# Kernel tuning notes

Measured on AMD Instinct MI355X. Metric: run time of the kernel, lower is better.

## Reference

```python
import jax, jax.numpy as jnp
import numpy as np

D_MODEL = 1024
NUM_HEADS = 16
HEAD_DIM = D_MODEL // NUM_HEADS  # 64
N = 1024
B = 8


def setup_inputs() -> dict:
    key = jax.random.key(0)
    ks = jax.random.split(key, 11)
    s = 0.02
    inp = {
        'query': jax.random.normal(ks[0], (B, D_MODEL, N), jnp.float32),
        'key':   jax.random.normal(ks[1], (B, D_MODEL, N), jnp.float32),
        'value': jax.random.normal(ks[2], (B, D_MODEL, N), jnp.float32),
        # 1x1 conv1d == linear over channel dim: weight [out, in], bias [out]
        'Wq': jax.random.normal(ks[3], (D_MODEL, D_MODEL), jnp.float32) * s,
        'bq': jax.random.normal(ks[4], (D_MODEL,), jnp.float32) * s,
        'Wk': jax.random.normal(ks[5], (D_MODEL, D_MODEL), jnp.float32) * s,
        'bk': jax.random.normal(ks[6], (D_MODEL,), jnp.float32) * s,
        'Wv': jax.random.normal(ks[7], (D_MODEL, D_MODEL), jnp.float32) * s,
        'bv': jax.random.normal(ks[8], (D_MODEL,), jnp.float32) * s,
        'Wm': jax.random.normal(ks[9], (D_MODEL, D_MODEL), jnp.float32) * s,
        'bm': jax.random.normal(ks[10], (D_MODEL,), jnp.float32) * s,
    }
    return inp


def _proj(W, b, x):
    # nn.Conv1d(kernel_size=1): out[b,o,n] = sum_i W[o,i] x[b,i,n] + b[o]
    return jnp.einsum('oi,bin->bon', W, x) + b[None, :, None]


def reference(query, key, value, Wq, bq, Wk, bk, Wv, bv, Wm, bm):
    Bd = query.shape[0]
    # view(B, dim, heads, N): channel axis split as (head_dim, num_heads)
    q = _proj(Wq, bq, query).reshape(Bd, HEAD_DIM, NUM_HEADS, -1)
    k = _proj(Wk, bk, key).reshape(Bd, HEAD_DIM, NUM_HEADS, -1)
    v = _proj(Wv, bv, value).reshape(Bd, HEAD_DIM, NUM_HEADS, -1)
    scale = 1.0 / (HEAD_DIM ** 0.5)
    scores = jnp.einsum('bdhn,bdhm->bhnm', q, k) * scale  # [B,H,N,N]
    prob = jax.nn.softmax(scores, axis=-1)
    x = jnp.einsum('bhnm,bdhm->bdhn', prob, v)  # [B,D,H,N]
    out = _proj(Wm, bm, x.reshape(Bd, HEAD_DIM * NUM_HEADS, -1))
    return out
```

## Files before the change

### kernel.cpp

```cpp
#include <hip/hip_runtime.h>

typedef __bf16 bf16x8 __attribute__((ext_vector_type(8)));
typedef __bf16 bf16x4 __attribute__((ext_vector_type(4)));
typedef float f32x4 __attribute__((ext_vector_type(4)));
typedef unsigned short u16;
typedef unsigned int u32;

__device__ __forceinline__ u16 f2bf(float f) {
  u32 u = __builtin_bit_cast(u32, f);
  u = (u + 0x7FFFu + ((u >> 16) & 1u)) >> 16;
  return (u16)u;
}

__device__ __forceinline__ void gload_lds16(const void* g, void* l) {
  __builtin_amdgcn_global_load_lds((const __attribute__((address_space(1))) void*)g,
                                   (__attribute__((address_space(3))) void*)l, 16, 0, 0);
}

__global__ __launch_bounds__(256) void transpose_cast(const float* __restrict__ src,
                                                      u16* __restrict__ dst) {
  __shared__ float T[64][68];
  int tid = threadIdx.x;
  int n0 = blockIdx.x * 64, i0 = blockIdx.y * 64;
  size_t boff = (size_t)blockIdx.z << 20;
  const float* s = src + boff;
  u16* d = dst + boff;
  int ir = tid >> 4, n4 = (tid & 15) * 4;
#pragma unroll
  for (int r = 0; r < 4; ++r) {
    int i_loc = ir + r * 16;
    float4 v = *(const float4*)(s + (size_t)(i0 + i_loc) * 1024 + n0 + n4);
    *(float4*)&T[i_loc][n4] = v;
  }
  __syncthreads();
  int nr = tid >> 3, i8 = (tid & 7) * 8;
#pragma unroll
  for (int r = 0; r < 2; ++r) {
    int n_loc = nr + r * 32;
    u32 pk[4];
#pragma unroll
    for (int j = 0; j < 4; ++j) {
      float f0 = T[i8 + 2 * j][n_loc];
      float f1 = T[i8 + 2 * j + 1][n_loc];
      pk[j] = (u32)f2bf(f0) | ((u32)f2bf(f1) << 16);
    }
    *(uint4*)(d + (size_t)(n0 + n_loc) * 1024 + i0 + i8) = make_uint4(pk[0], pk[1], pk[2], pk[3]);
  }
}

__global__ __launch_bounds__(256) void cast_weights(const float* __restrict__ Wq,
                                                    const float* __restrict__ Wk,
                                                    const float* __restrict__ Wv,
                                                    const float* __restrict__ Wm,
                                                    u16* __restrict__ out) {
  int w = blockIdx.y;
  const float* src = (w == 0) ? Wq : (w == 1) ? Wk : (w == 2) ? Wv : Wm;
  u16* dst = out + ((size_t)w << 20);
  int o = blockIdx.x;
  int c4 = threadIdx.x * 4;
  float f[4];
  if (w < 3) {
    float4 v = *(const float4*)(src + (size_t)o * 1024 + c4);
    f[0] = v.x; f[1] = v.y; f[2] = v.z; f[3] = v.w;
  } else {
#pragma unroll
    for (int j = 0; j < 4; ++j) {
      int cp = c4 + j;
      f[j] = src[(size_t)o * 1024 + (cp & 63) * 16 + (cp >> 6)];
    }
  }
  u32 p0 = (u32)f2bf(f[0]) | ((u32)f2bf(f[1]) << 16);
  u32 p1 = (u32)f2bf(f[2]) | ((u32)f2bf(f[3]) << 16);
  *(uint2*)(dst + (size_t)o * 1024 + c4) = make_uint2(p0, p1);
}

template <int EPI>
__global__ __launch_bounds__(512, 2) void gemm4b(const u16* __restrict__ A,
                                                 const u16* __restrict__ B,
                                                 const float* __restrict__ bias,
                                                 void* __restrict__ Out, float escale) {
  __shared__ u16 LD[49152];
  int tid = threadIdx.x;
  int wave = tid >> 6, l = tid & 63, ln = l & 15, g = l >> 4;
  int wm = wave >> 2, wn = wave & 3;
  int bid = blockIdx.x;
  int mt = (bid >> 3) & 7;
  int nt = ((bid & 7) << 2) | (bid >> 6);
  int c0 = mt * 128, n0 = nt * 256;

  int R = tid >> 3, sl = tid & 7;
  int v = sl ^ (R & 7);
  int sa = v >> 2, sg = v & 3;
  const u16* aSrc = A + (size_t)(c0 + 2 * R + sa) * 1024 + sg * 8;
  const u16* bSrc0 = B + (size_t)(n0 + 2 * R + sa) * 1024 + sg * 8;
  const u16* bSrc1 = B + (size_t)(n0 + 128 + 2 * R + sa) * 1024 + sg * 8;

  int slr = ((((ln & 1) << 2) | g) ^ ((ln >> 1) & 7)) * 8;
  int laneA = (wm * 32 + (ln >> 1)) * 64 + slr;
  int laneB = (wn * 32 + (ln >> 1)) * 64 + slr;

  f32x4 acc[4][4] = {};

#define STAGE(buf, kt)                                                   \
  do {                                                                   \
    gload_lds16(aSrc + (kt) * 32, &LD[(buf) * 4096 + tid * 8]);          \
    gload_lds16(bSrc0 + (kt) * 32, &LD[16384 + (buf) * 8192 + tid * 8]); \
    gload_lds16(bSrc1 + (kt) * 32,                                       \
                &LD[16384 + (buf) * 8192 + 4096 + tid * 8]);             \
  } while (0)

  STAGE(0, 0);
  STAGE(1, 1);
  STAGE(2, 2);

#pragma unroll
  for (int t = 0; t < 32; ++t) {
    if (t < 30)
      asm volatile("s_waitcnt vmcnt(6)" ::: "memory");
    else if (t == 30)
      asm volatile("s_waitcnt vmcnt(3)" ::: "memory");
    else
      asm volatile("s_waitcnt vmcnt(0)" ::: "memory");
    asm volatile("s_barrier" ::: "memory");
    if (t <= 28) STAGE((t + 3) & 3, t + 3);
    const int ab = (t & 3) * 4096;
    const int bb = 16384 + (t & 3) * 8192;
    bf16x8 af[4], bfr[4];
#pragma unroll
    for (int mm = 0; mm < 4; ++mm) af[mm] = *(const bf16x8*)&LD[ab + laneA + mm * 512];
#pragma unroll
    for (int nn = 0; nn < 4; ++nn) bfr[nn] = *(const bf16x8*)&LD[bb + laneB + nn * 512];
    __builtin_amdgcn_s_setprio(1);
#pragma unroll
    for (int mm = 0; mm < 4; ++mm)
#pragma unroll
      for (int nn = 0; nn < 4; ++nn)
        acc[mm][nn] = __builtin_amdgcn_mfma_f32_16x16x32_bf16(af[mm], bfr[nn], acc[mm][nn], 0, 0, 0);
    __builtin_amdgcn_s_setprio(0);
  }
#undef STAGE

  int D0 = (c0 >> 4) + wm * 4;
#pragma unroll
  for (int nn = 0; nn < 4; ++nn) {
    size_t ng = (size_t)n0 + wn * 64 + nn * 16 + ln;
#pragma unroll
    for (int r = 0; r < 4; ++r) {
      int h = g * 4 + r;
      if (EPI == 0) {
        bf16x4 pk;
#pragma unroll
        for (int mm = 0; mm < 4; ++mm) {
          int c = c0 + wm * 64 + mm * 16 + h;
          pk[mm] = (__bf16)((acc[mm][nn][r] + bias[c]) * escale);
        }
        *(bf16x4*)((u16*)Out + ng * 1024 + (size_t)h * 64 + D0) = pk;
      } else {
        size_t b = ng >> 10, n = ng & 1023;
#pragma unroll
        for (int mm = 0; mm < 4; ++mm) {
          int c = c0 + wm * 64 + mm * 16 + h;
          float val = (acc[mm][nn][r] + bias[c]) * escale;
          if (EPI == 1) {
            int d = D0 + mm;
            ((u16*)Out)[((b * 16 + h) * 64 + d) * 1024 + n] = f2bf(val);
          } else {
            ((float*)Out)[(b << 20) + (size_t)c * 1024 + n] = val;
          }
        }
      }
    }
  }
}

__global__ __launch_bounds__(256) void attn_kernel(const u16* __restrict__ Qh,
                                                   const u16* __restrict__ Kh,
                                                   const u16* __restrict__ Vt,
                                                   u16* __restrict__ Xh) {
  __shared__ u16 Ks[2][4096];
  __shared__ u16 Vs[2][4096];
  __shared__ u16 Ps[8][16 * 72];
  int tid = threadIdx.x;
  int w = tid >> 6, l = tid & 63, ln = l & 15, g = l >> 4;
  int id = blockIdx.x;
  int qp = (id & 63) >> 3;
  int bh = ((id >> 6) << 3) | (id & 7);
  size_t b = bh >> 4;
  int h = bh & 15;
  const u16* Qg = Qh + (b << 20) + (h << 6);
  const u16* Kg = Kh + (b << 20) + (h << 6);
  const u16* Vg = Vt + ((size_t)bh << 16);
  u16* Og = Xh + (b << 20) + (h << 6);

  bf16x8 qf[2][2];
#pragma unroll
  for (int t = 0; t < 2; ++t)
#pragma unroll
    for (int kk = 0; kk < 2; ++kk)
      qf[t][kk] = *(const bf16x8*)(Qg + (size_t)(qp * 128 + t * 64 + w * 16 + ln) * 1024 + kk * 32 + g * 8);

  int lr = l >> 3;
  int sw8 = ((l & 7) ^ lr) << 3;
  int r0 = w * 16 + lr, r1 = r0 + 8;
  const u16* kS0 = Kg + (size_t)r0 * 1024 + sw8;
  const u16* kS1 = Kg + (size_t)r1 * 1024 + sw8;
  const u16* vS0 = Vg + (size_t)r0 * 1024 + sw8;
  const u16* vS1 = Vg + (size_t)r1 * 1024 + sw8;

  f32x4 xacc[2][4] = {};
  float lacc[2] = {0.f, 0.f};

  gload_lds16(kS0, &Ks[0][(w * 2) * 512]);
  gload_lds16(kS1, &Ks[0][(w * 2 + 1) * 512]);
  gload_lds16(vS0, &Vs[0][(w * 2) * 512]);
  gload_lds16(vS1, &Vs[0][(w * 2 + 1) * 512]);
  __syncthreads();

  int sx = ln & 7;
  int cur = 0;
  for (int kt = 0; kt < 16; ++kt) {
    if (kt < 15) {
      int nxt = cur ^ 1;
      gload_lds16(kS0 + (size_t)(kt + 1) * 65536, &Ks[nxt][(w * 2) * 512]);
      gload_lds16(kS1 + (size_t)(kt + 1) * 65536, &Ks[nxt][(w * 2 + 1) * 512]);
      gload_lds16(vS0 + (kt + 1) * 64, &Vs[nxt][(w * 2) * 512]);
      gload_lds16(vS1 + (kt + 1) * 64, &Vs[nxt][(w * 2 + 1) * 512]);
    }
    bf16x8 kf[2][4], vf[2][4];
#pragma unroll
    for (int kk = 0; kk < 2; ++kk)
#pragma unroll
      for (int f = 0; f < 4; ++f) {
        int slot = (((kk << 2) + g) ^ sx) << 3;
        kf[kk][f] = *(const bf16x8*)&Ks[cur][(f * 16 + ln) * 64 + slot];
        vf[kk][f] = *(const bf16x8*)&Vs[cur][(f * 16 + ln) * 64 + slot];
      }
    f32x4 sacc[2][4] = {};
#pragma unroll
    for (int t = 0; t < 2; ++t)
#pragma unroll
      for (int kk = 0; kk < 2; ++kk)
#pragma unroll
        for (int f = 0; f < 4; ++f)
          sacc[t][f] = __builtin_amdgcn_mfma_f32_16x16x32_bf16(kf[kk][f], qf[t][kk], sacc[t][f], 0, 0, 0);
#pragma unroll
    for (int t = 0; t < 2; ++t) {
      u16* PsW = Ps[w * 2 + t];
#pragma unroll
      for (int f = 0; f < 4; ++f) {
        float p0 = __builtin_amdgcn_exp2f(sacc[t][f][0]);
        float p1 = __builtin_amdgcn_exp2f(sacc[t][f][1]);
        float p2 = __builtin_amdgcn_exp2f(sacc[t][f][2]);
        float p3 = __builtin_amdgcn_exp2f(sacc[t][f][3]);
        lacc[t] += (p0 + p1) + (p2 + p3);
        bf16x4 pb;
        pb[0] = (__bf16)p0; pb[1] = (__bf16)p1; pb[2] = (__bf16)p2; pb[3] = (__bf16)p3;
        *(bf16x4*)&PsW[ln * 72 + (f << 4) + (g << 2)] = pb;
      }
    }
#pragma unroll
    for (int t = 0; t < 2; ++t) {
      const u16* PsR = Ps[w * 2 + t];
#pragma unroll
      for (int kk = 0; kk < 2; ++kk) {
        bf16x8 pf = *(const bf16x8*)&PsR[ln * 72 + (kk << 5) + (g << 3)];
#pragma unroll
        for (int fd = 0; fd < 4; ++fd)
          xacc[t][fd] = __builtin_amdgcn_mfma_f32_16x16x32_bf16(pf, vf[kk][fd], xacc[t][fd], 0, 0, 0);
      }
    }
    __syncthreads();
    cur ^= 1;
  }

#pragma unroll
  for (int t = 0; t < 2; ++t) {
    float lt = lacc[t];
    lt += __shfl_xor(lt, 16);
    lt += __shfl_xor(lt, 32);
    float il[4];
#pragma unroll
    for (int r = 0; r < 4; ++r) il[r] = 1.0f / __shfl(lt, g * 4 + r);
#pragma unroll
    for (int fd = 0; fd < 4; ++fd)
#pragma unroll
      for (int r = 0; r < 4; ++r) {
        int nq = qp * 128 + t * 64 + w * 16 + g * 4 + r;
        Og[(size_t)nq * 1024 + fd * 16 + ln] = f2bf(xacc[t][fd][r] * il[r]);
      }
  }
}

extern "C" void kernel_launch(void* const* d_in, const int* in_sizes, int n_in,
                              void* d_out, int out_size, void* d_ws, size_t ws_size,
                              hipStream_t stream) {
  const float* q  = (const float*)d_in[0];
  const float* k  = (const float*)d_in[1];
  const float* v  = (const float*)d_in[2];
  const float* Wq = (const float*)d_in[3];
  const float* bq = (const float*)d_in[4];
  const float* Wk = (const float*)d_in[5];
  const float* bk = (const float*)d_in[6];
  const float* Wv = (const float*)d_in[7];
  const float* bv = (const float*)d_in[8];
  const float* Wm = (const float*)d_in[9];
  const float* bm = (const float*)d_in[10];

  char* ws = (char*)d_ws;
  u16* Wbf = (u16*)ws;
  u16* Qh  = (u16*)(ws + (8ull << 20));
  u16* Kh  = (u16*)(ws + (24ull << 20));
  u16* Vt  = (u16*)(ws + (40ull << 20));
  u16* Xt  = (u16*)(ws + (56ull << 20));

  cast_weights<<<dim3(1024, 4, 1), 256, 0, stream>>>(Wq, Wk, Wv, Wm, Wbf);

  dim3 tg(16, 16, 8);
  const float qscale = 0.125f * 1.44269504088896340736f;

  transpose_cast<<<tg, 256, 0, stream>>>(q, Xt);
  gemm4b<0><<<256, 512, 0, stream>>>(Wbf, Xt, bq, Qh, qscale);
  transpose_cast<<<tg, 256, 0, stream>>>(k, Xt);
  gemm4b<0><<<256, 512, 0, stream>>>(Wbf + (1u << 20), Xt, bk, Kh, 1.0f);
  transpose_cast<<<tg, 256, 0, stream>>>(v, Xt);
  gemm4b<1><<<256, 512, 0, stream>>>(Wbf + (2u << 20), Xt, bv, Vt, 1.0f);

  attn_kernel<<<1024, 256, 0, stream>>>(Qh, Kh, Vt, Xt);

  gemm4b<2><<<256, 512, 0, stream>>>(Wbf + (3u << 20), Xt, bm, d_out, 1.0f);
}
```

Before: 190.6 us.

## Batch Q/K/V transpose-cast and projection GEMMs into single launches

```diff
diff --git a/kernel.cpp b/kernel.cpp
--- a/kernel.cpp
+++ b/kernel.cpp
@@ -15,6 +15,42 @@
 __device__ __forceinline__ void gload_lds16(const void* g, void* l) {
   __builtin_amdgcn_global_load_lds((const __attribute__((address_space(1))) void*)g,
                                    (__attribute__((address_space(3))) void*)l, 16, 0, 0);
+}
+
+__global__ __launch_bounds__(256) void transpose_cast3(const float* __restrict__ q,
+                                                       const float* __restrict__ k,
+                                                       const float* __restrict__ v,
+                                                       u16* __restrict__ X3) {
+  __shared__ float T[64][68];
+  int tid = threadIdx.x;
+  int n0 = blockIdx.x * 64, i0 = blockIdx.y * 64;
+  int z = blockIdx.z;
+  int which = z >> 3, b = z & 7;
+  const float* src = (which == 0) ? q : (which == 1) ? k : v;
+  size_t boff = (size_t)b << 20;
+  const float* s = src + boff;
+  u16* d = X3 + ((size_t)which << 23) + boff;
+  int ir = tid >> 4, n4 = (tid & 15) * 4;
+#pragma unroll
+  for (int r = 0; r < 4; ++r) {
+    int i_loc = ir + r * 16;
+    float4 vv = *(const float4*)(s + (size_t)(i0 + i_loc) * 1024 + n0 + n4);
+    *(float4*)&T[i_loc][n4] = vv;
+  }
+  __syncthreads();
+  int nr = tid >> 3, i8 = (tid & 7) * 8;
+#pragma unroll
+  for (int r = 0; r < 2; ++r) {
+    int n_loc = nr + r * 32;
+    u32 pk[4];
+#pragma unroll
+    for (int j = 0; j < 4; ++j) {
+      float f0 = T[i8 + 2 * j][n_loc];
+      float f1 = T[i8 + 2 * j + 1][n_loc];
+      pk[j] = (u32)f2bf(f0) | ((u32)f2bf(f1) << 16);
+    }
+    *(uint4*)(d + (size_t)(n0 + n_loc) * 1024 + i0 + i8) = make_uint4(pk[0], pk[1], pk[2], pk[3]);
+  }
 }
 
 __global__ __launch_bounds__(256) void transpose_cast(const float* __restrict__ src,
@@ -74,12 +110,11 @@
   *(uint2*)(dst + (size_t)o * 1024 + c4) = make_uint2(p0, p1);
 }
 
-template <int EPI>
-__global__ __launch_bounds__(512, 2) void gemm4b(const u16* __restrict__ A,
-                                                 const u16* __restrict__ B,
-                                                 const float* __restrict__ bias,
-                                                 void* __restrict__ Out, float escale) {
-  __shared__ u16 LD[49152];
+__device__ __forceinline__ void gemm_body(const u16* __restrict__ A,
+                                          const u16* __restrict__ B,
+                                          const float* __restrict__ bias,
+                                          void* __restrict__ Out, float escale,
+                                          int epi, u16* LD) {
   int tid = threadIdx.x;
   int wave = tid >> 6, l = tid & 63, ln = l & 15, g = l >> 4;
   int wm = wave >> 2, wn = wave & 3;
@@ -147,7 +182,7 @@
 #pragma unroll
     for (int r = 0; r < 4; ++r) {
       int h = g * 4 + r;
-      if (EPI == 0) {
+      if (epi == 0) {
         bf16x4 pk;
 #pragma unroll
         for (int mm = 0; mm < 4; ++mm) {
@@ -161,7 +196,7 @@
         for (int mm = 0; mm < 4; ++mm) {
           int c = c0 + wm * 64 + mm * 16 + h;
           float val = (acc[mm][nn][r] + bias[c]) * escale;
-          if (EPI == 1) {
+          if (epi == 1) {
             int d = D0 + mm;
             ((u16*)Out)[((b * 16 + h) * 64 + d) * 1024 + n] = f2bf(val);
           } else {
@@ -171,6 +206,34 @@
       }
     }
   }
+}
+
+template <int EPI>
+__global__ __launch_bounds__(512, 2) void gemm4b(const u16* __restrict__ A,
+                                                 const u16* __restrict__ B,
+                                                 const float* __restrict__ bias,
+                                                 void* __restrict__ Out, float escale) {
+  __shared__ u16 LD[49152];
+  gemm_body(A, B, bias, Out, escale, EPI, LD);
+}
+
+__global__ __launch_bounds__(512, 2) void gemm_qkv(const u16* __restrict__ Wbf,
+                                                   const u16* __restrict__ X3,
+                                                   const float* __restrict__ bq,
+                                                   const float* __restrict__ bk,
+                                                   const float* __restrict__ bv,
+                                                   u16* __restrict__ Qh,
+                                                   u16* __restrict__ Kh,
+                                                   u16* __restrict__ Vt, float qscale) {
+  __shared__ u16 LD[49152];
+  int z = blockIdx.y;
+  const u16* A = Wbf + ((size_t)z << 20);
+  const u16* B = X3 + ((size_t)z << 23);
+  const float* bias = (z == 0) ? bq : (z == 1) ? bk : bv;
+  void* Out = (z == 0) ? (void*)Qh : (z == 1) ? (void*)Kh : (void*)Vt;
+  float escale = (z == 0) ? qscale : 1.0f;
+  int epi = (z == 2) ? 1 : 0;
+  gemm_body(A, B, bias, Out, escale, epi, LD);
 }
 
 __global__ __launch_bounds__(256) void attn_kernel(const u16* __restrict__ Qh,
@@ -311,21 +374,26 @@
   u16* Qh  = (u16*)(ws + (8ull << 20));
   u16* Kh  = (u16*)(ws + (24ull << 20));
   u16* Vt  = (u16*)(ws + (40ull << 20));
-  u16* Xt  = (u16*)(ws + (56ull << 20));
+  u16* X3  = (u16*)(ws + (56ull << 20));
 
   cast_weights<<<dim3(1024, 4, 1), 256, 0, stream>>>(Wq, Wk, Wv, Wm, Wbf);
 
-  dim3 tg(16, 16, 8);
   const float qscale = 0.125f * 1.44269504088896340736f;
 
-  transpose_cast<<<tg, 256, 0, stream>>>(q, Xt);
-  gemm4b<0><<<256, 512, 0, stream>>>(Wbf, Xt, bq, Qh, qscale);
-  transpose_cast<<<tg, 256, 0, stream>>>(k, Xt);
-  gemm4b<0><<<256, 512, 0, stream>>>(Wbf + (1u << 20), Xt, bk, Kh, 1.0f);
-  transpose_cast<<<tg, 256, 0, stream>>>(v, Xt);
-  gemm4b<1><<<256, 512, 0, stream>>>(Wbf + (2u << 20), Xt, bv, Vt, 1.0f);
-
-  attn_kernel<<<1024, 256, 0, stream>>>(Qh, Kh, Vt, Xt);
-
-  gemm4b<2><<<256, 512, 0, stream>>>(Wbf + (3u << 20), Xt, bm, d_out, 1.0f);
-}
+  if (ws_size >= (104ull << 20)) {
+    transpose_cast3<<<dim3(16, 16, 24), 256, 0, stream>>>(q, k, v, X3);
+    gemm_qkv<<<dim3(256, 3), 512, 0, stream>>>(Wbf, X3, bq, bk, bv, Qh, Kh, Vt, qscale);
+  } else {
+    dim3 tg(16, 16, 8);
+    transpose_cast<<<tg, 256, 0, stream>>>(q, X3);
+    gemm4b<0><<<256, 512, 0, stream>>>(Wbf, X3, bq, Qh, qscale);
+    transpose_cast<<<tg, 256, 0, stream>>>(k, X3);
+    gemm4b<0><<<256, 512, 0, stream>>>(Wbf + (1u << 20), X3, bk, Kh, 1.0f);
+    transpose_cast<<<tg, 256, 0, stream>>>(v, X3);
+    gemm4b<1><<<256, 512, 0, stream>>>(Wbf + (2u << 20), X3, bv, Vt, 1.0f);
+  }
+
+  attn_kernel<<<1024, 256, 0, stream>>>(Qh, Kh, Vt, X3);
+
+  gemm4b<2><<<256, 512, 0, stream>>>(Wbf + (3u << 20), X3, bm, d_out, 1.0f);
+}
```

Measured after the change: 185.6 us. 2.6% less time.
